# Optimization experiments

Hardware: AMD Instinct MI355X
Metric: run time of the kernel (lower is better)

## Reference

```python
import jax, jax.numpy as jnp
import numpy as np
from math import log2, ceil

HEADS, DIM_HEAD, BLOCK, EPS = 16, 64, 16, 1e-8


def setup_inputs() -> dict:
    key = jax.random.key(0)
    k1, k2, k3, k4 = jax.random.split(key, 4)
    b, n, dim = 4, 4096, 1024
    inner = HEADS * DIM_HEAD
    return {
        "x": jax.random.normal(k1, (b, n, dim), jnp.float32),
        "w_qkv": jax.random.normal(k2, (inner * 3, dim), jnp.float32) * 0.02,
        "w_out": jax.random.normal(k3, (dim, inner), jnp.float32) * 0.02,
        "b_out": jax.random.normal(k4, (dim,), jnp.float32) * 0.02,
    }


def reference(x, w_qkv, w_out, b_out):
    b, n, dim = x.shape
    pad_to_len = 2 ** ceil(log2(n))
    if pad_to_len != n:
        x = jnp.pad(x, ((0, 0), (0, pad_to_len - n), (0, 0)))
    qkv = x @ w_qkv.T  # torch Linear (no bias): weight is [out, in]
    q, k, v = jnp.split(qkv, 3, axis=-1)

    def split_heads(t):
        return t.reshape(b, pad_to_len, HEADS, DIM_HEAD).transpose(0, 2, 1, 3).reshape(b * HEADS, pad_to_len, DIM_HEAD)

    q = split_heads(q) * DIM_HEAD ** -0.5
    k = split_heads(k)
    v = split_heads(v)

    num_levels = int(log2(pad_to_len // BLOCK)) - 1
    # hierarchical coarsening: q,k averaged over pairs, v summed over pairs
    qkvs = [(q, k, v)]
    for _ in range(num_levels):
        q = q.reshape(q.shape[0], -1, 2, DIM_HEAD).mean(2)
        k = k.reshape(k.shape[0], -1, 2, DIM_HEAD).mean(2)
        v = v.reshape(v.shape[0], -1, 2, DIM_HEAD).sum(2)
        qkvs.append((q, k, v))

    neg_max = -jnp.finfo(x.dtype).max
    idx = jnp.arange(pad_to_len)
    Ysum = jnp.zeros((b * HEADS, pad_to_len, DIM_HEAD), x.dtype)
    Asum = jnp.zeros((b * HEADS, pad_to_len), x.dtype)

    for lvl, (ql, kl, vl) in enumerate(qkvs):
        B = ql.shape[0]
        nb = ql.shape[1] // BLOCK  # number of blocks at this level
        ql = ql.reshape(B, nb, BLOCK, DIM_HEAD)
        kl = kl.reshape(B, nb, BLOCK, DIM_HEAD)
        vl = vl.reshape(B, nb, BLOCK, DIM_HEAD)
        if lvl == 0:
            # finest level: causal diagonal block attention
            S = jnp.einsum('bnid,bnjd->bnij', ql, kl)
            S = jnp.where(jnp.triu(jnp.ones((BLOCK, BLOCK), bool), 1), neg_max, S)
            S = S - S.max(-1, keepdims=True)
            A = jnp.exp(S)
            y = jnp.einsum('bnij,bnjd->bnid', A, vl).reshape(B, pad_to_len, DIM_HEAD)
            Av = A.sum(-1).reshape(B, pad_to_len)
        else:
            # off-diagonal: second block of each pair attends to first block of pair
            q2 = ql.reshape(B, nb // 2, 2, BLOCK, DIM_HEAD)[:, :, 1]
            k1b = kl.reshape(B, nb // 2, 2, BLOCK, DIM_HEAD)[:, :, 0]  # flip_every_two then take [:,1]
            v1b = vl.reshape(B, nb // 2, 2, BLOCK, DIM_HEAD)[:, :, 0]
            S = jnp.einsum('bnid,bnjd->bnij', q2, k1b)
            S = S - S.max(-1, keepdims=True)
            A = jnp.exp(S)
            y = jnp.einsum('bnij,bnjd->bnid', A, v1b)  # [B, nb/2, BLOCK, d]
            Av = A.sum(-1)
            # zero-pad first block of each pair, flatten blocks back to sequence
            y = jnp.pad(y[:, :, None], ((0, 0), (0, 0), (1, 0), (0, 0), (0, 0))).reshape(B, -1, DIM_HEAD)
            Av = jnp.pad(Av[:, :, None], ((0, 0), (0, 0), (1, 0), (0, 0))).reshape(B, -1)
            # expand coarsened positions to full resolution (consecutive repeats)
            y = jnp.repeat(y, 2 ** lvl, axis=1)
            Av = jnp.repeat(Av, 2 ** lvl, axis=1)
        # causal keep-mask: max original index inside the coarsened key group <= query index
        seq_key = (idx >> lvl << lvl) + (2 ** lvl - 1)
        keep = seq_key <= idx  # at lvl=0 seq_key == idx -> keep all
        Ysum = Ysum + jnp.where(keep[None, :, None], y, 0.0)
        Asum = Asum + jnp.where(keep[None, :], Av, 0.0)

    out = Ysum / (Asum + EPS)[..., None]
    out = out.reshape(b, HEADS, pad_to_len, DIM_HEAD).transpose(0, 2, 1, 3).reshape(b, pad_to_len, HEADS * DIM_HEAD)
    out = out @ w_out.T + b_out
    return out[:, :n]
```

## Files before the change

### kernel.cpp

```cpp
#include <hip/hip_runtime.h>

typedef __bf16 bf16_t;
typedef __attribute__((ext_vector_type(8))) __bf16 bf16x8;
typedef __attribute__((ext_vector_type(4))) float f32x4;

#define MFMA(a,b,c) __builtin_amdgcn_mfma_f32_16x16x32_bf16(a,b,c,0,0,0)

static __device__ __forceinline__ unsigned short f2bfbits(float f){
  unsigned int u = __builtin_bit_cast(unsigned int, f);
  return (unsigned short)((u + 0x7FFFu + ((u >> 16) & 1u)) >> 16);
}
static __device__ __forceinline__ float bits2f(unsigned int b){
  return __builtin_bit_cast(float, b << 16);
}
static __device__ __forceinline__ void gl_lds16(const void* g, void* l){
  __builtin_amdgcn_global_load_lds(
      (const __attribute__((address_space(1))) void*)(g),
      (__attribute__((address_space(3))) void*)(l), 16, 0, 0);
}
static __device__ __forceinline__ void unpack8(uint4 raw, float* f){
  f[0]=bits2f(raw.x&0xFFFFu); f[1]=bits2f(raw.x>>16);
  f[2]=bits2f(raw.y&0xFFFFu); f[3]=bits2f(raw.y>>16);
  f[4]=bits2f(raw.z&0xFFFFu); f[5]=bits2f(raw.z>>16);
  f[6]=bits2f(raw.w&0xFFFFu); f[7]=bits2f(raw.w>>16);
}

__global__ __launch_bounds__(256) void cvt_f32_bf16(const float* __restrict__ in,
                                                    unsigned short* __restrict__ out,
                                                    long n4){
  const long stride = (long)gridDim.x * 256;
  for (long i = (long)blockIdx.x * 256 + threadIdx.x; i < n4; i += stride){
    float4 v = *(const float4*)(in + i * 4);
    unsigned long long pack = (unsigned long long)f2bfbits(v.x)
      | ((unsigned long long)f2bfbits(v.y) << 16)
      | ((unsigned long long)f2bfbits(v.z) << 32)
      | ((unsigned long long)f2bfbits(v.w) << 48);
    *(unsigned long long*)(out + i * 4) = pack;
  }
}

template<int MODE>
__global__ __launch_bounds__(512, 2) void gemm256(
    const unsigned short* __restrict__ A, const unsigned short* __restrict__ B,
    const int K, const int nbx,
    unsigned short* __restrict__ oq, unsigned short* __restrict__ ok2, unsigned short* __restrict__ ov,
    float* __restrict__ outp, const float* __restrict__ bias)
{
  __shared__ char lds[131072];
  const int t = threadIdx.x;
  const int lane = t & 63, wid = t >> 6;
  const int wr = wid >> 2, wc = wid & 3;
  const int r16 = lane & 15, g = lane >> 4;

  const int nb = gridDim.x, cpx = nb >> 3;
  const int lin = (blockIdx.x & 7) * cpx + (blockIdx.x >> 3);
  const int by = lin / nbx, bx = lin - by * nbx;
  const long row0 = (long)by * 256, col0 = (long)bx * 256;

  const unsigned short* gA[4]; const unsigned short* gB[4];
  int ldsoff[4];
  #pragma unroll
  for (int r2 = 0; r2 < 4; ++r2){
    const int flat = r2*512 + t;
    const int row = flat >> 3, slot = flat & 7;
    const int slotg = slot ^ (row & 7);
    gA[r2] = A + (row0 + row) * K + slotg*8;
    gB[r2] = B + (col0 + row) * K + slotg*8;
    ldsoff[r2] = (r2*512 + wid*64) * 16;
  }

  f32x4 acc[8][4];
  #pragma unroll
  for (int m = 0; m < 8; ++m)
    #pragma unroll
    for (int n = 0; n < 4; ++n)
      acc[m][n] = (f32x4){0.f, 0.f, 0.f, 0.f};

  const int nk = K >> 6;

  #pragma unroll
  for (int r2 = 0; r2 < 4; ++r2){
    gl_lds16(gA[r2], lds + ldsoff[r2]);
    gl_lds16(gB[r2], lds + 32768 + ldsoff[r2]);
  }

  for (int kt = 0; kt < nk; ++kt){
    char* ldsA = lds + (kt & 1)*65536;
    char* ldsB = ldsA + 32768;
    if (kt + 1 < nk){
      char* nA = lds + ((kt+1)&1)*65536;
      const int koff = (kt+1)*64;
      #pragma unroll
      for (int r2 = 0; r2 < 4; ++r2){
        gl_lds16(gA[r2] + koff, nA + ldsoff[r2]);
        gl_lds16(gB[r2] + koff, nA + 32768 + ldsoff[r2]);
      }
      asm volatile("s_waitcnt vmcnt(8)" ::: "memory");
    } else {
      asm volatile("s_waitcnt vmcnt(0)" ::: "memory");
    }
    __builtin_amdgcn_s_barrier();
    __builtin_amdgcn_sched_barrier(0);

    bf16x8 bfrag[4][2];
    #pragma unroll
    for (int n = 0; n < 4; ++n)
      #pragma unroll
      for (int kk = 0; kk < 2; ++kk){
        const int row = wc*64 + n*16 + r16;
        bfrag[n][kk] = *(const bf16x8*)(ldsB + row*128 + (((kk*4 + g) ^ (row & 7)) * 16));
      }
    #pragma unroll
    for (int mp = 0; mp < 4; ++mp){
      bf16x8 afr[2][2];
      #pragma unroll
      for (int mi = 0; mi < 2; ++mi)
        #pragma unroll
        for (int kk = 0; kk < 2; ++kk){
          const int row = wr*128 + (mp*2 + mi)*16 + r16;
          afr[mi][kk] = *(const bf16x8*)(ldsA + row*128 + (((kk*4 + g) ^ (row & 7)) * 16));
        }
      __builtin_amdgcn_s_setprio(1);
      #pragma unroll
      for (int mi = 0; mi < 2; ++mi)
        #pragma unroll
        for (int n = 0; n < 4; ++n)
          #pragma unroll
          for (int kk = 0; kk < 2; ++kk)
            acc[mp*2 + mi][n] = MFMA(afr[mi][kk], bfrag[n][kk], acc[mp*2 + mi][n]);
      __builtin_amdgcn_s_setprio(0);
    }
    __builtin_amdgcn_sched_barrier(0);
    __builtin_amdgcn_s_barrier();
  }

  if (MODE == 0){
    __syncthreads();
    const int which = (int)(col0 >> 10);
    const int h = (int)((col0 & 1023) >> 6) + wc;
    const float sc = (which == 0) ? 0.125f : 1.0f;
    unsigned short* st = (unsigned short*)lds + wid*8192;
    #pragma unroll
    for (int pass = 0; pass < 2; ++pass){
      #pragma unroll
      for (int mm = 0; mm < 4; ++mm)
        #pragma unroll
        for (int n = 0; n < 4; ++n)
          #pragma unroll
          for (int q2 = 0; q2 < 4; ++q2)
            st[(mm*16 + g*4 + q2)*72 + n*16 + r16] = f2bfbits(acc[pass*4 + mm][n][q2] * sc);
      const long prow0 = row0 + wr*128 + pass*64;
      if (which < 2){
        unsigned short* dst = (which == 0) ? oq : ok2;
        #pragma unroll
        for (int rd = 0; rd < 8; ++rd){
          const int rl = rd*8 + (lane >> 3);
          const int gr = lane & 7;
          uint4 v = *(const uint4*)&st[rl*72 + gr*8];
          const long ii = prow0 + rl;
          const int b_ = (int)(ii >> 12), pos = (int)(ii & 4095);
          *(uint4*)&dst[(((long)b_*16 + h)*4096 + pos)*64 + gr*8] = v;
        }
      } else {
        #pragma unroll
        for (int rd = 0; rd < 8; ++rd){
          const int blk = rd >> 1;
          const int d = (rd & 1)*32 + (lane >> 1);
          const int kkh = lane & 1;
          unsigned short tmp[8];
          #pragma unroll
          for (int j = 0; j < 8; ++j)
            tmp[j] = st[(blk*16 + kkh*8 + j)*72 + d];
          uint4 v;
          v.x = (unsigned int)tmp[0] | ((unsigned int)tmp[1] << 16);
          v.y = (unsigned int)tmp[2] | ((unsigned int)tmp[3] << 16);
          v.z = (unsigned int)tmp[4] | ((unsigned int)tmp[5] << 16);
          v.w = (unsigned int)tmp[6] | ((unsigned int)tmp[7] << 16);
          const long posblk = (prow0 >> 4) + blk;
          const int b_ = (int)(posblk >> 8), blkg = (int)(posblk & 255);
          *(uint4*)&ov[(((long)b_*16 + h)*256 + blkg)*1024 + d*16 + kkh*8] = v;
        }
      }
      __builtin_amdgcn_sched_barrier(0);
    }
  } else {
    #pragma unroll
    for (int n = 0; n < 4; ++n){
      const long j = col0 + wc*64 + n*16 + r16;
      const float bi = bias[j];
      #pragma unroll
      for (int m = 0; m < 8; ++m){
        const long ib = row0 + wr*128 + m*16 + g*4;
        #pragma unroll
        for (int q2 = 0; q2 < 4; ++q2)
          outp[(ib + q2)*1024 + j] = acc[m][n][q2] + bi;
      }
    }
  }
}

__global__ __launch_bounds__(256) void coarsen(
    const unsigned short* __restrict__ q0, const unsigned short* __restrict__ k0,
    const unsigned short* __restrict__ vt0,
    unsigned short* __restrict__ qch, unsigned short* __restrict__ kch,
    unsigned short* __restrict__ vch)
{
  __shared__ float Abuf[128*64];
  __shared__ float Bbuf[64*64];
  const int t = threadIdx.x;
  const int chunk = blockIdx.x;
  const int bh = blockIdx.y;
  const int arr = blockIdx.z;
  if (arr < 2){
    const unsigned short* src = (arr == 0) ? q0 : k0;
    const long sbase = ((long)bh*4096 + (long)chunk*128) * 64;
    #pragma unroll
    for (int it = 0; it < 4; ++it){
      const int idx = it*2048 + t*8;
      uint4 raw = *(const uint4*)(src + sbase + idx);
      float f[8]; unpack8(raw, f);
      #pragma unroll
      for (int j = 0; j < 8; ++j) Abuf[idx + j] = f[j];
    }
  } else {
    const long sbase = ((long)bh*256 + (long)chunk*8) * 1024;
    #pragma unroll
    for (int it = 0; it < 4; ++it){
      const int flat = it*2048 + t*8;
      const int blk = flat >> 10, rem = flat & 1023;
      const int d = rem >> 4, kk0 = rem & 15;
      uint4 raw = *(const uint4*)(vt0 + sbase + flat);
      float f[8]; unpack8(raw, f);
      #pragma unroll
      for (int j = 0; j < 8; ++j) Abuf[(blk*16 + kk0 + j)*64 + d] = f[j];
    }
  }
  __syncthreads();
  float* cur = Abuf; float* nxt = Bbuf;
  int rows = 128;
  const int Spre[8] = {0, 0, 1024, 1536, 1792, 1920, 1984, 2016};
  for (int l = 1; l <= 7; ++l){
    rows >>= 1;
    const int P = 2048 >> l;
    const long base = (long)Spre[l] * 4096;
    for (int e = t; e < rows*64; e += 256){
      const int p = e >> 6, d = e & 63;
      const float a = cur[(2*p)*64 + d], b2 = cur[(2*p + 1)*64 + d];
      const float val = (arr == 2) ? (a + b2) : 0.5f*(a + b2);
      nxt[e] = val;
      const int pl = chunk*rows + p;
      const int cb = pl >> 4, ci = cb >> 1;
      const unsigned short bv = f2bfbits(val);
      if (arr == 0){
        if (cb & 1) qch[base + ((long)bh*P + ci*16 + (pl & 15))*64 + d] = bv;
      } else if (arr == 1){
        if (!(cb & 1)) kch[base + ((long)bh*P + ci*16 + (pl & 15))*64 + d] = bv;
      } else {
        if (!(cb & 1)) vch[base + (long)bh*P*64 + ci*1024 + d*16 + (pl & 15)] = bv;
      }
    }
    __syncthreads();
    float* tmp = cur; cur = nxt; nxt = tmp;
  }
}

__global__ __launch_bounds__(256) void attn_fused(
    const unsigned short* __restrict__ q0, const unsigned short* __restrict__ k0,
    const unsigned short* __restrict__ vt0,
    const unsigned short* __restrict__ qch, const unsigned short* __restrict__ kch,
    const unsigned short* __restrict__ vch,
    unsigned short* __restrict__ ybf)
{
  const int lane = threadIdx.x & 63;
  const int w = threadIdx.x >> 6;
  const int B0 = blockIdx.x * 4 + w;
  const int bh = blockIdx.y;
  const int b_ = bh >> 4, h = bh & 15;
  const int r = lane & 15, g = lane >> 4;
  __shared__ float accs_all[4][16*64];
  __shared__ float denoms_all[4][16];
  float* accs = accs_all[w];
  float* denoms = denoms_all[w];

  {
    const long base = ((long)bh*4096 + (long)B0*16) * 64;
    const bf16x8 ka0 = *(const bf16x8*)(k0 + base + r*64 + g*8);
    const bf16x8 ka1 = *(const bf16x8*)(k0 + base + r*64 + g*8 + 32);
    const bf16x8 qb0 = *(const bf16x8*)(q0 + base + r*64 + g*8);
    const bf16x8 qb1 = *(const bf16x8*)(q0 + base + r*64 + g*8 + 32);
    f32x4 s = {0.f,0.f,0.f,0.f};
    s = MFMA(ka0, qb0, s);
    s = MFMA(ka1, qb1, s);

    float p[4];
    float mx = -3.402823466e38f;
    #pragma unroll
    for (int j = 0; j < 4; ++j){
      const int c = g*4 + j;
      p[j] = (c <= r) ? s[j] : -3.402823466e38f;
      mx = fmaxf(mx, p[j]);
    }
    mx = fmaxf(mx, __shfl_xor(mx, 16));
    mx = fmaxf(mx, __shfl_xor(mx, 32));
    float rs = 0.f;
    #pragma unroll
    for (int j = 0; j < 4; ++j){
      const int c = g*4 + j;
      p[j] = (c <= r) ? __expf(p[j] - mx) : 0.f;
      rs += p[j];
    }
    rs += __shfl_xor(rs, 16);
    rs += __shfl_xor(rs, 32);

    float x16[4], x32[4], x48[4];
    #pragma unroll
    for (int j = 0; j < 4; ++j){
      x16[j] = __shfl_xor(p[j], 16);
      x32[j] = __shfl_xor(p[j], 32);
      x48[j] = __shfl_xor(p[j], 48);
    }
    bf16x8 af;
    #pragma unroll
    for (int j = 0; j < 4; ++j){
      const float lo = (g == 0) ? p[j]   : (g == 1) ? x48[j] : 0.f;
      const float hi = (g == 0) ? x16[j] : (g == 1) ? x32[j] : 0.f;
      af[j]   = (bf16_t)lo;
      af[j+4] = (bf16_t)hi;
    }
    const unsigned short* vt = vt0 + ((long)bh*256 + B0) * 1024;
    #pragma unroll
    for (int nb = 0; nb < 4; ++nb){
      bf16x8 bv;
      #pragma unroll
      for (int j = 0; j < 8; ++j) bv[j] = (bf16_t)0.f;
      if (g < 2) bv = *(const bf16x8*)(vt + (nb*16 + r)*16 + g*8);
      f32x4 y = {0.f,0.f,0.f,0.f};
      y = MFMA(af, bv, y);
      #pragma unroll
      for (int q2 = 0; q2 < 4; ++q2)
        accs[(g*4 + q2)*64 + nb*16 + r] = y[q2];
    }
    if (g == 0) denoms[r] = rs;
  }

  const int Spre[8] = {0, 0, 1024, 1536, 1792, 1920, 1984, 2016};
  for (int l = 1; l <= 7; ++l){
    int nr, lo, cb;
    if (l <= 4){
      nr = 16 >> l;
      lo = (B0 & ((1 << l) - 1)) << (4 - l);
      cb = B0 >> l;
    } else {
      const int m = 1 << (l - 4);
      if ((B0 & (m - 1)) != m - 1) continue;
      const int qrow = ((B0 + 1) >> (l - 4)) - 1;
      cb = qrow >> 4; lo = qrow & 15; nr = 1;
    }
    if (!(cb & 1)) continue;
    const int ci = cb >> 1;
    const int P = 2048 >> l;
    const long base = (long)Spre[l] * 4096;
    const long qb_base = base + ((long)bh*P + ci*16) * 64;
    const long kv_base = base + (long)bh*P*64 + (long)ci*1024;

    const bf16x8 ka0 = *(const bf16x8*)(kch + qb_base + r*64 + g*8);
    const bf16x8 ka1 = *(const bf16x8*)(kch + qb_base + r*64 + g*8 + 32);
    const bf16x8 qb0 = *(const bf16x8*)(qch + qb_base + r*64 + g*8);
    const bf16x8 qb1 = *(const bf16x8*)(qch + qb_base + r*64 + g*8 + 32);
    f32x4 s = {0.f,0.f,0.f,0.f};
    s = MFMA(ka0, qb0, s);
    s = MFMA(ka1, qb1, s);

    float p[4];
    float mx = fmaxf(fmaxf(s[0], s[1]), fmaxf(s[2], s[3]));
    mx = fmaxf(mx, __shfl_xor(mx, 16));
    mx = fmaxf(mx, __shfl_xor(mx, 32));
    float rs = 0.f;
    #pragma unroll
    for (int j = 0; j < 4; ++j){ p[j] = __expf(s[j] - mx); rs += p[j]; }
    rs += __shfl_xor(rs, 16);
    rs += __shfl_xor(rs, 32);

    float x16[4], x32[4], x48[4];
    #pragma unroll
    for (int j = 0; j < 4; ++j){
      x16[j] = __shfl_xor(p[j], 16);
      x32[j] = __shfl_xor(p[j], 32);
      x48[j] = __shfl_xor(p[j], 48);
    }
    bf16x8 af;
    #pragma unroll
    for (int j = 0; j < 4; ++j){
      const float lo2 = (g == 0) ? p[j]   : (g == 1) ? x48[j] : 0.f;
      const float hi2 = (g == 0) ? x16[j] : (g == 1) ? x32[j] : 0.f;
      af[j]   = (bf16_t)lo2;
      af[j+4] = (bf16_t)hi2;
    }
    #pragma unroll
    for (int nb = 0; nb < 4; ++nb){
      bf16x8 bv;
      #pragma unroll
      for (int j = 0; j < 8; ++j) bv[j] = (bf16_t)0.f;
      if (g < 2) bv = *(const bf16x8*)(vch + kv_base + (nb*16 + r)*16 + g*8);
      f32x4 y = {0.f,0.f,0.f,0.f};
      y = MFMA(af, bv, y);
      #pragma unroll
      for (int q2 = 0; q2 < 4; ++q2){
        const int row = g*4 + q2;
        if (row >= lo && row < lo + nr){
          const int ii = (((cb*16 + row + 1) << l) - 1) - (B0 << 4);
          accs[ii*64 + nb*16 + r] += y[q2];
        }
      }
    }
    if (g == 0 && r >= lo && r < lo + nr){
      const int ii = (((cb*16 + r + 1) << l) - 1) - (B0 << 4);
      denoms[ii] += rs;
    }
  }

  const int row = lane >> 2, d0 = (lane & 3) * 16;
  const float inv = 1.f / (denoms[row] + 1e-8f);
  unsigned int wv[8];
  #pragma unroll
  for (int j2 = 0; j2 < 8; ++j2){
    const float a = accs[row*64 + d0 + 2*j2]      * inv;
    const float b2 = accs[row*64 + d0 + 2*j2 + 1] * inv;
    wv[j2] = (unsigned int)f2bfbits(a) | ((unsigned int)f2bfbits(b2) << 16);
  }
  uint4* dst = (uint4*)(ybf + ((long)b_*4096 + B0*16 + row)*1024 + h*64 + d0);
  dst[0] = make_uint4(wv[0], wv[1], wv[2], wv[3]);
  dst[1] = make_uint4(wv[4], wv[5], wv[6], wv[7]);
}

extern "C" void kernel_launch(void* const* d_in, const int* in_sizes, int n_in,
                              void* d_out, int out_size, void* d_ws, size_t ws_size,
                              hipStream_t stream){
  const float* x    = (const float*)d_in[0];
  const float* wqkv = (const float*)d_in[1];
  const float* wout = (const float*)d_in[2];
  const float* bout = (const float*)d_in[3];
  float* out = (float*)d_out;
  char* ws = (char*)d_ws;

  unsigned short* wqb = (unsigned short*)(ws + 0L);
  unsigned short* wob = (unsigned short*)(ws + 6291456L);
  unsigned short* xb  = (unsigned short*)(ws + 8388608L);
  unsigned short* q0  = (unsigned short*)(ws + 41943040L);
  unsigned short* k0  = (unsigned short*)(ws + 75497472L);
  unsigned short* vt0 = (unsigned short*)(ws + 109051904L);
  unsigned short* qch = (unsigned short*)(ws + 142606336L);
  unsigned short* kch = (unsigned short*)(ws + 159252480L);
  unsigned short* vch = (unsigned short*)(ws + 175898624L);
  unsigned short* ybf = xb;

  cvt_f32_bf16<<<2048, 256, 0, stream>>>(x,    xb,  (long)16384*1024/4);
  cvt_f32_bf16<<<512,  256, 0, stream>>>(wqkv, wqb, (long)3072*1024/4);
  cvt_f32_bf16<<<256,  256, 0, stream>>>(wout, wob, (long)1024*1024/4);

  gemm256<0><<<768, 512, 0, stream>>>(xb, wqb, 1024, 12, q0, k0, vt0, nullptr, nullptr);
  coarsen<<<dim3(32,64,3), 256, 0, stream>>>(q0, k0, vt0, qch, kch, vch);
  attn_fused<<<dim3(64,64), 256, 0, stream>>>(q0, k0, vt0, qch, kch, vch, ybf);
  gemm256<1><<<256, 512, 0, stream>>>(ybf, wob, 1024, 4, nullptr, nullptr, nullptr, out, bout);
}
```

Baseline: 305.0 us.

## Merge conversion kernels, deepen GEMM pipeline, pad coarsen LDS and coalesce V stores

The three f32-to-bf16 conversion launches become one kernel that picks its source by index range, which removes two launches. The GEMM main loop now uses K-steps of 32 with a four-slot LDS ring, loading three stages ahead. Loads are issued in half-stages between two MFMA halves, with a new swizzle for the 64-byte rows. The coarsen kernel pads its LDS rows to 65 floats to avoid bank conflicts and writes the transposed V output in a second pass with contiguous stores. The added barriers and waitcnt logic in the GEMM loop are complex and could introduce stalls or races.

```diff
diff --git a/kernel.cpp b/kernel.cpp
--- a/kernel.cpp
+++ b/kernel.cpp
@@ -25,17 +25,25 @@
   f[6]=bits2f(raw.w&0xFFFFu); f[7]=bits2f(raw.w>>16);
 }
 
-__global__ __launch_bounds__(256) void cvt_f32_bf16(const float* __restrict__ in,
-                                                    unsigned short* __restrict__ out,
-                                                    long n4){
+__global__ __launch_bounds__(256) void cvt_all(const float* __restrict__ x,
+                                               const float* __restrict__ wqkv,
+                                               const float* __restrict__ wout,
+                                               unsigned short* __restrict__ xb,
+                                               unsigned short* __restrict__ wqb,
+                                               unsigned short* __restrict__ wob){
+  const long n4 = 5242880;
   const long stride = (long)gridDim.x * 256;
   for (long i = (long)blockIdx.x * 256 + threadIdx.x; i < n4; i += stride){
-    float4 v = *(const float4*)(in + i * 4);
+    const float* in; unsigned short* out; long e;
+    if (i < 4194304){ in = x; out = xb; e = i; }
+    else if (i < 4980736){ in = wqkv; out = wqb; e = i - 4194304; }
+    else { in = wout; out = wob; e = i - 4980736; }
+    float4 v = *(const float4*)(in + e * 4);
     unsigned long long pack = (unsigned long long)f2bfbits(v.x)
       | ((unsigned long long)f2bfbits(v.y) << 16)
       | ((unsigned long long)f2bfbits(v.z) << 32)
       | ((unsigned long long)f2bfbits(v.w) << 48);
-    *(unsigned long long*)(out + i * 4) = pack;
+    *(unsigned long long*)(out + e * 4) = pack;
   }
 }
 
@@ -57,15 +65,15 @@
   const int by = lin / nbx, bx = lin - by * nbx;
   const long row0 = (long)by * 256, col0 = (long)bx * 256;
 
-  const unsigned short* gA[4]; const unsigned short* gB[4];
-  int ldsoff[4];
+  const unsigned short* gA[2]; const unsigned short* gB[2];
+  int ldsoff[2];
   #pragma unroll
-  for (int r2 = 0; r2 < 4; ++r2){
+  for (int r2 = 0; r2 < 2; ++r2){
     const int flat = r2*512 + t;
-    const int row = flat >> 3, slot = flat & 7;
-    const int slotg = slot ^ (row & 7);
-    gA[r2] = A + (row0 + row) * K + slotg*8;
-    gB[r2] = B + (col0 + row) * K + slotg*8;
+    const int row = flat >> 2;
+    const int sg = (flat & 3) ^ ((row >> 1) & 3);
+    gA[r2] = A + (row0 + row) * K + sg*8;
+    gB[r2] = B + (col0 + row) * K + sg*8;
     ldsoff[r2] = (r2*512 + wid*64) * 16;
   }
 
@@ -76,63 +84,73 @@
     for (int n = 0; n < 4; ++n)
       acc[m][n] = (f32x4){0.f, 0.f, 0.f, 0.f};
 
-  const int nk = K >> 6;
-
-  #pragma unroll
-  for (int r2 = 0; r2 < 4; ++r2){
-    gl_lds16(gA[r2], lds + ldsoff[r2]);
-    gl_lds16(gB[r2], lds + 32768 + ldsoff[r2]);
-  }
-
-  for (int kt = 0; kt < nk; ++kt){
-    char* ldsA = lds + (kt & 1)*65536;
-    char* ldsB = ldsA + 32768;
-    if (kt + 1 < nk){
-      char* nA = lds + ((kt+1)&1)*65536;
-      const int koff = (kt+1)*64;
-      #pragma unroll
-      for (int r2 = 0; r2 < 4; ++r2){
-        gl_lds16(gA[r2] + koff, nA + ldsoff[r2]);
-        gl_lds16(gB[r2] + koff, nA + 32768 + ldsoff[r2]);
-      }
+  const int nk = K >> 5;
+
+  #define STAGE_H(s, half) do{                                  \
+    const long koff = (long)(s) * 32;                           \
+    char* sb = lds + ((s) & 3) * 32768;                         \
+    gl_lds16(gA[half] + koff, sb + ldsoff[half]);               \
+    gl_lds16(gB[half] + koff, sb + 16384 + ldsoff[half]);       \
+  }while(0)
+
+  STAGE_H(0,0); STAGE_H(0,1);
+  STAGE_H(1,0); STAGE_H(1,1);
+  STAGE_H(2,0); STAGE_H(2,1);
+  asm volatile("s_waitcnt vmcnt(8)" ::: "memory");
+  __builtin_amdgcn_s_barrier();
+
+  for (int i = 0; i < nk; ++i){
+    const char* sl = lds + (i & 3) * 32768;
+    bf16x8 bfr[4], afr[8];
+    #pragma unroll
+    for (int n = 0; n < 4; ++n){
+      const int br = wc*64 + n*16 + r16;
+      bfr[n] = *(const bf16x8*)(sl + 16384 + br*64 + ((g ^ ((br >> 1) & 3)) << 4));
+    }
+    #pragma unroll
+    for (int m = 0; m < 4; ++m){
+      const int ar = wr*128 + m*16 + r16;
+      afr[m] = *(const bf16x8*)(sl + ar*64 + ((g ^ ((ar >> 1) & 3)) << 4));
+    }
+    if (i + 3 < nk) STAGE_H(i + 3, 0);
+    __builtin_amdgcn_s_barrier();
+    asm volatile("s_waitcnt lgkmcnt(0)" ::: "memory");
+    __builtin_amdgcn_sched_barrier(0);
+    __builtin_amdgcn_s_setprio(1);
+    #pragma unroll
+    for (int m = 0; m < 4; ++m)
+      #pragma unroll
+      for (int n = 0; n < 4; ++n)
+        acc[m][n] = MFMA(afr[m], bfr[n], acc[m][n]);
+    __builtin_amdgcn_s_setprio(0);
+    __builtin_amdgcn_s_barrier();
+
+    #pragma unroll
+    for (int m = 4; m < 8; ++m){
+      const int ar = wr*128 + m*16 + r16;
+      afr[m] = *(const bf16x8*)(sl + ar*64 + ((g ^ ((ar >> 1) & 3)) << 4));
+    }
+    if (i + 3 < nk){
+      STAGE_H(i + 3, 1);
       asm volatile("s_waitcnt vmcnt(8)" ::: "memory");
-    } else {
+    } else if (i == nk - 3){
+      asm volatile("s_waitcnt vmcnt(4)" ::: "memory");
+    } else if (i == nk - 2){
       asm volatile("s_waitcnt vmcnt(0)" ::: "memory");
     }
     __builtin_amdgcn_s_barrier();
+    asm volatile("s_waitcnt lgkmcnt(0)" ::: "memory");
     __builtin_amdgcn_sched_barrier(0);
-
-    bf16x8 bfrag[4][2];
-    #pragma unroll
-    for (int n = 0; n < 4; ++n)
-      #pragma unroll
-      for (int kk = 0; kk < 2; ++kk){
-        const int row = wc*64 + n*16 + r16;
-        bfrag[n][kk] = *(const bf16x8*)(ldsB + row*128 + (((kk*4 + g) ^ (row & 7)) * 16));
-      }
-    #pragma unroll
-    for (int mp = 0; mp < 4; ++mp){
-      bf16x8 afr[2][2];
-      #pragma unroll
-      for (int mi = 0; mi < 2; ++mi)
-        #pragma unroll
-        for (int kk = 0; kk < 2; ++kk){
-          const int row = wr*128 + (mp*2 + mi)*16 + r16;
-          afr[mi][kk] = *(const bf16x8*)(ldsA + row*128 + (((kk*4 + g) ^ (row & 7)) * 16));
-        }
-      __builtin_amdgcn_s_setprio(1);
-      #pragma unroll
-      for (int mi = 0; mi < 2; ++mi)
-        #pragma unroll
-        for (int n = 0; n < 4; ++n)
-          #pragma unroll
-          for (int kk = 0; kk < 2; ++kk)
-            acc[mp*2 + mi][n] = MFMA(afr[mi][kk], bfrag[n][kk], acc[mp*2 + mi][n]);
-      __builtin_amdgcn_s_setprio(0);
-    }
-    __builtin_amdgcn_sched_barrier(0);
+    __builtin_amdgcn_s_setprio(1);
+    #pragma unroll
+    for (int m = 4; m < 8; ++m)
+      #pragma unroll
+      for (int n = 0; n < 4; ++n)
+        acc[m][n] = MFMA(afr[m], bfr[n], acc[m][n]);
+    __builtin_amdgcn_s_setprio(0);
     __builtin_amdgcn_s_barrier();
   }
+  #undef STAGE_H
 
   if (MODE == 0){
     __syncthreads();
@@ -205,8 +223,8 @@
     unsigned short* __restrict__ qch, unsigned short* __restrict__ kch,
     unsigned short* __restrict__ vch)
 {
-  __shared__ float Abuf[128*64];
-  __shared__ float Bbuf[64*64];
+  __shared__ float Abuf[128*65];
+  __shared__ float Bbuf[64*65];
   const int t = threadIdx.x;
   const int chunk = blockIdx.x;
   const int bh = blockIdx.y;
@@ -219,8 +237,9 @@
       const int idx = it*2048 + t*8;
       uint4 raw = *(const uint4*)(src + sbase + idx);
       float f[8]; unpack8(raw, f);
-      #pragma unroll
-      for (int j = 0; j < 8; ++j) Abuf[idx + j] = f[j];
+      const int rowb = idx >> 6, colb = idx & 63;
+      #pragma unroll
+      for (int j = 0; j < 8; ++j) Abuf[rowb*65 + colb + j] = f[j];
     }
   } else {
     const long sbase = ((long)bh*256 + (long)chunk*8) * 1024;
@@ -232,7 +251,7 @@
       uint4 raw = *(const uint4*)(vt0 + sbase + flat);
       float f[8]; unpack8(raw, f);
       #pragma unroll
-      for (int j = 0; j < 8; ++j) Abuf[(blk*16 + kk0 + j)*64 + d] = f[j];
+      for (int j = 0; j < 8; ++j) Abuf[(blk*16 + kk0 + j)*65 + d] = f[j];
     }
   }
   __syncthreads();
@@ -245,21 +264,30 @@
     const long base = (long)Spre[l] * 4096;
     for (int e = t; e < rows*64; e += 256){
       const int p = e >> 6, d = e & 63;
-      const float a = cur[(2*p)*64 + d], b2 = cur[(2*p + 1)*64 + d];
+      const float a = cur[(2*p)*65 + d], b2 = cur[(2*p + 1)*65 + d];
       const float val = (arr == 2) ? (a + b2) : 0.5f*(a + b2);
-      nxt[e] = val;
+      nxt[p*65 + d] = val;
       const int pl = chunk*rows + p;
       const int cb = pl >> 4, ci = cb >> 1;
-      const unsigned short bv = f2bfbits(val);
       if (arr == 0){
-        if (cb & 1) qch[base + ((long)bh*P + ci*16 + (pl & 15))*64 + d] = bv;
+        if (cb & 1) qch[base + ((long)bh*P + ci*16 + (pl & 15))*64 + d] = f2bfbits(val);
       } else if (arr == 1){
-        if (!(cb & 1)) kch[base + ((long)bh*P + ci*16 + (pl & 15))*64 + d] = bv;
-      } else {
-        if (!(cb & 1)) vch[base + (long)bh*P*64 + ci*1024 + d*16 + (pl & 15)] = bv;
+        if (!(cb & 1)) kch[base + ((long)bh*P + ci*16 + (pl & 15))*64 + d] = f2bfbits(val);
+      } else if (rows < 16){
+        if (!(cb & 1)) vch[base + (long)bh*P*64 + ci*1024 + d*16 + (pl & 15)] = f2bfbits(val);
       }
     }
     __syncthreads();
+    if (arr == 2 && rows >= 16){
+      const int nblk = rows >> 4;
+      for (int oe = t; oe < nblk*1024; oe += 256){
+        const int bl = oe >> 10, rem = oe & 1023;
+        const int cb = chunk*nblk + bl;
+        if (cb & 1) continue;
+        const int d = rem >> 4, kk = rem & 15;
+        vch[base + (long)bh*P*64 + (long)(cb>>1)*1024 + rem] = f2bfbits(nxt[(bl*16 + kk)*65 + d]);
+      }
+    }
     float* tmp = cur; cur = nxt; nxt = tmp;
   }
 }
@@ -454,9 +482,7 @@
   unsigned short* vch = (unsigned short*)(ws + 175898624L);
   unsigned short* ybf = xb;
 
-  cvt_f32_bf16<<<2048, 256, 0, stream>>>(x,    xb,  (long)16384*1024/4);
-  cvt_f32_bf16<<<512,  256, 0, stream>>>(wqkv, wqb, (long)3072*1024/4);
-  cvt_f32_bf16<<<256,  256, 0, stream>>>(wout, wob, (long)1024*1024/4);
+  cvt_all<<<2048, 256, 0, stream>>>(x, wqkv, wout, xb, wqb, wob);
 
   gemm256<0><<<768, 512, 0, stream>>>(xb, wqb, 1024, 12, q0, k0, vt0, nullptr, nullptr);
   coarsen<<<dim3(32,64,3), 256, 0, stream>>>(q0, k0, vt0, qch, kch, vch);
```

After: 308.3 us. About the same (+1.1%).
